# Kernel optimization log

Measured on AMD Instinct MI355X. Metric: run time of the kernel, lower is better.

The kernel has to match this reference:

```python
import jax, jax.numpy as jnp
import numpy as np

B, S, E = 2, 2048, 2048
H, KV, D = 16, 4, 128
G = H // KV  # query heads per kv head
THETA = 10000.0


def setup_inputs() -> dict:
    key = jax.random.key(0)
    ks = jax.random.split(key, 5)
    scale = 0.02
    return {
        "x": jax.random.normal(ks[0], (B, S, E), dtype=jnp.float32),
        "Wq": jax.random.normal(ks[1], (E, H * D), dtype=jnp.float32) * scale,
        "Wk": jax.random.normal(ks[2], (E, KV * D), dtype=jnp.float32) * scale,
        "Wv": jax.random.normal(ks[3], (E, KV * D), dtype=jnp.float32) * scale,
        "Wo": jax.random.normal(ks[4], (E, E), dtype=jnp.float32) * scale,
    }


def _rope_tables(seq_len, head_dim, theta):
    inv_freq = 1.0 / theta ** (jnp.arange(0, head_dim, 2, dtype=jnp.float32) / head_dim)
    t = jnp.arange(seq_len, dtype=jnp.float32)
    freqs = jnp.outer(t, inv_freq)  # [S, D/2]
    cos = jnp.concatenate([jnp.cos(freqs), jnp.cos(freqs)], axis=-1)  # [S, D]
    sin = jnp.concatenate([jnp.sin(freqs), jnp.sin(freqs)], axis=-1)
    return cos, sin


def _apply_rope(x, cos, sin):
    # x: [B, h, S, D]; cos/sin: [S, D] broadcast over batch/heads
    d2 = x.shape[-1] // 2
    x1, x2 = x[..., :d2], x[..., d2:]
    rotated = jnp.concatenate([-x2, x1], axis=-1)
    return x * cos + rotated * sin


def reference(x, Wq, Wk, Wv, Wo):
    b, s, _ = x.shape
    q = (x @ Wq).reshape(b, s, H, D).transpose(0, 2, 1, 3)   # [B,H,S,D]
    k = (x @ Wk).reshape(b, s, KV, D).transpose(0, 2, 1, 3)  # [B,KV,S,D]
    v = (x @ Wv).reshape(b, s, KV, D).transpose(0, 2, 1, 3)

    cos, sin = _rope_tables(s, D, THETA)
    q = _apply_rope(q, cos, sin)
    k = _apply_rope(k, cos, sin)

    # GQA: q head h attends to kv head h // G (repeat_interleave order)
    qg = q.reshape(b, KV, G, s, D)
    scores = jnp.einsum("bkgsd,bktd->bkgst", qg, k) / jnp.sqrt(jnp.asarray(D, x.dtype))
    causal = jnp.tril(jnp.ones((s, s), dtype=bool))
    scores = jnp.where(causal, scores, jnp.asarray(-jnp.inf, scores.dtype))
    attn = jax.nn.softmax(scores, axis=-1)
    out = jnp.einsum("bkgst,bktd->bkgsd", attn, v)  # [B,KV,G,S,D]
    out = out.reshape(b, H, s, D).transpose(0, 2, 1, 3).reshape(b, s, H * D)
    return out @ Wo
```

## Files before the change

kernel.cpp:

```cpp
#include <hip/hip_runtime.h>
#include <stdint.h>

#define B_ 2
#define S_ 2048
#define E_ 2048
#define H_ 16
#define KV_ 4
#define D_ 128
#define G_ (H_ / KV_)
#define M_ (B_ * S_)

typedef unsigned short u16;
typedef unsigned int u32;
typedef __bf16 bf16x8 __attribute__((ext_vector_type(8)));
typedef float f32x4 __attribute__((ext_vector_type(4)));

__device__ __forceinline__ u16 f2bf(float f) {
  __bf16 h = (__bf16)f;
  return *(u16*)&h;
}
__device__ __forceinline__ float bf2f(u16 x) {
  return __uint_as_float(((u32)x) << 16);
}
__device__ __forceinline__ void store_c(u16* p, float v) { *p = f2bf(v); }
__device__ __forceinline__ void store_c(float* p, float v) { *p = v; }

__device__ __forceinline__ void gload_lds16(const u16* g, u16* lds) {
  __builtin_amdgcn_global_load_lds((const __attribute__((address_space(1))) u32*)g,
                                   (__attribute__((address_space(3))) u32*)lds,
                                   16, 0, 0);
}

__global__ __launch_bounds__(256) void convert_fp32_bf16(const float4* __restrict__ x,
                                                         uint2* __restrict__ o, int n4) {
  int i = blockIdx.x * 256 + threadIdx.x;
  if (i >= n4) return;
  float4 v = x[i];
  uint2 r;
  r.x = (u32)f2bf(v.x) | ((u32)f2bf(v.y) << 16);
  r.y = (u32)f2bf(v.z) | ((u32)f2bf(v.w) << 16);
  o[i] = r;
}

__global__ __launch_bounds__(256) void transpose_conv_w(const float* __restrict__ W,
                                                        u16* __restrict__ Wt,
                                                        int Kdim, int Ndim) {
  __shared__ float tile[32][33];
  int n0 = blockIdx.x * 32, k0 = blockIdx.y * 32;
  int tx = threadIdx.x, ty = threadIdx.y;
#pragma unroll
  for (int i = 0; i < 4; i++) {
    int r = ty + i * 8;
    tile[r][tx] = W[(size_t)(k0 + r) * Ndim + n0 + tx];
  }
  __syncthreads();
#pragma unroll
  for (int i = 0; i < 4; i++) {
    int r = ty + i * 8;
    Wt[(size_t)(n0 + r) * Kdim + k0 + tx] = f2bf(tile[tx][r]);
  }
}

__global__ __launch_bounds__(256) void transpose_v(const u16* __restrict__ V,
                                                   u16* __restrict__ Vt) {
  __shared__ u16 tile[32][33];
  int bkv = blockIdx.z;
  int b = bkv / KV_, kv = bkv % KV_;
  int s0 = blockIdx.x * 32, d0 = blockIdx.y * 32;
  int tx = threadIdx.x, ty = threadIdx.y;
#pragma unroll
  for (int i = 0; i < 4; i++) {
    int r = ty + i * 8;
    tile[r][tx] = V[((size_t)((b * S_ + s0 + r) * KV_ + kv)) * D_ + d0 + tx];
  }
  __syncthreads();
#pragma unroll
  for (int i = 0; i < 4; i++) {
    int r = ty + i * 8;
    Vt[((size_t)(b * KV_ + kv) * D_ + d0 + r) * S_ + s0 + tx] = tile[tx][r];
  }
}

__global__ __launch_bounds__(256) void rope_k_repack(const u16* __restrict__ Kin,
                                                     u16* __restrict__ Kp, int total) {
  int idx = blockIdx.x * 256 + threadIdx.x;
  if (idx >= total) return;
  int d = idx & 63;
  int rem = idx >> 6;
  int kv = rem % KV_;
  int row = rem / KV_;
  int b = row >> 11;
  int spos = row & (S_ - 1);
  size_t src = ((size_t)row * KV_ + kv) * D_ + d;
  float x0 = bf2f(Kin[src]);
  float x1 = bf2f(Kin[src + 64]);
  float ang = (float)spos * expf(-0.14391156831212787f * (float)d);
  float sn, cs;
  sincosf(ang, &sn, &cs);
  size_t dst = ((size_t)((b * KV_ + kv) * S_ + spos)) * D_ + d;
  Kp[dst]      = f2bf(x0 * cs - x1 * sn);
  Kp[dst + 64] = f2bf(x1 * cs + x0 * sn);
}

template <typename CT>
__device__ __forceinline__ void gemm256_body(const u16* __restrict__ A,
                                             const u16* __restrict__ Bt,
                                             CT* __restrict__ C,
                                             int Kdim, int Ndim, int m0, int n0) {
  extern __shared__ __align__(16) u16 smem[];
  const int tid  = threadIdx.x;
  const int lane = tid & 63;
  const int wave = tid >> 6;
  const int wm   = wave >> 2;
  const int wn   = wave & 3;
  const int bh   = wn >> 1;
  const int nb   = (wn & 1) * 64;
  const int quad = lane >> 4, lm = lane & 15;

  int soff[2], sldb[2];
#pragma unroll
  for (int i = 0; i < 2; i++) {
    int cc  = i * 512 + tid;
    int row = cc >> 3;
    int q   = (cc & 7) ^ (row & 7);
    soff[i] = row * Kdim + q * 8;
    sldb[i] = (i * 512 + wave * 64) * 8;
  }
  auto STAGE = [&](const u16* g, u16* l) {
    gload_lds16(g + soff[0], l + sldb[0]);
    gload_lds16(g + soff[1], l + sldb[1]);
  };

  int cs0 = ((0 + quad) ^ (lm & 7)) * 8;
  int cs1 = ((4 + quad) ^ (lm & 7)) * 8;

  const u16* Ag = A  + (size_t)m0 * Kdim;
  const u16* Bg = Bt + (size_t)n0 * Kdim;
  const size_t hstep = (size_t)128 * Kdim;

  f32x4 acc[8][4];
  f32x4 zero = {0.f, 0.f, 0.f, 0.f};
#pragma unroll
  for (int m = 0; m < 8; m++)
#pragma unroll
    for (int n = 0; n < 4; n++) acc[m][n] = zero;

  const int NKT = Kdim >> 6;

  STAGE(Bg,             smem + 32768 + 0 * 8192);
  STAGE(Ag,             smem + 0 * 8192);
  STAGE(Ag + hstep,     smem + 1 * 8192);
  STAGE(Bg + hstep,     smem + 32768 + 1 * 8192);
  STAGE(Bg + 64,        smem + 32768 + 2 * 8192);
  STAGE(Ag + 64,        smem + 2 * 8192);
  STAGE(Ag + hstep + 64, smem + 3 * 8192);
  asm volatile("s_waitcnt vmcnt(6)" ::: "memory");
  __builtin_amdgcn_s_barrier();

  for (int kt = 0; kt < NKT; ++kt) {
    const int cur = kt & 1;
    const u16* regA = smem + (cur * 2 + wm) * 8192;
    const u16* regB = smem + 32768 + (cur * 2 + bh) * 8192;
    bf16x8 af[4][2], bf[4][2];

#pragma unroll
    for (int n = 0; n < 4; n++) {
      bf[n][0] = *(const bf16x8*)(regB + (nb + n * 16 + lm) * 64 + cs0);
      bf[n][1] = *(const bf16x8*)(regB + (nb + n * 16 + lm) * 64 + cs1);
    }
#pragma unroll
    for (int m = 0; m < 4; m++) {
      af[m][0] = *(const bf16x8*)(regA + (m * 16 + lm) * 64 + cs0);
      af[m][1] = *(const bf16x8*)(regA + (m * 16 + lm) * 64 + cs1);
    }
    if (kt + 1 < NKT)
      STAGE(Bg + hstep + (size_t)(kt + 1) * 64,
            smem + 32768 + (((kt + 1) & 1) * 2 + 1) * 8192);
    asm volatile("s_waitcnt lgkmcnt(0)" ::: "memory");
    __builtin_amdgcn_s_barrier();
    __builtin_amdgcn_s_setprio(1);
#pragma unroll
    for (int m = 0; m < 4; m++)
#pragma unroll
      for (int n = 0; n < 2; n++) {
        acc[m][n] = __builtin_amdgcn_mfma_f32_16x16x32_bf16(af[m][0], bf[n][0], acc[m][n], 0, 0, 0);
        acc[m][n] = __builtin_amdgcn_mfma_f32_16x16x32_bf16(af[m][1], bf[n][1], acc[m][n], 0, 0, 0);
      }
    __builtin_amdgcn_s_setprio(0);
    __builtin_amdgcn_s_barrier();

    if (kt + 2 < NKT)
      STAGE(Bg + (size_t)(kt + 2) * 64, smem + 32768 + (cur * 2 + 0) * 8192);
    __builtin_amdgcn_s_barrier();
    __builtin_amdgcn_s_setprio(1);
#pragma unroll
    for (int m = 0; m < 4; m++)
#pragma unroll
      for (int n = 2; n < 4; n++) {
        acc[m][n] = __builtin_amdgcn_mfma_f32_16x16x32_bf16(af[m][0], bf[n][0], acc[m][n], 0, 0, 0);
        acc[m][n] = __builtin_amdgcn_mfma_f32_16x16x32_bf16(af[m][1], bf[n][1], acc[m][n], 0, 0, 0);
      }
    __builtin_amdgcn_s_setprio(0);
    __builtin_amdgcn_s_barrier();

#pragma unroll
    for (int m = 0; m < 4; m++) {
      af[m][0] = *(const bf16x8*)(regA + ((m + 4) * 16 + lm) * 64 + cs0);
      af[m][1] = *(const bf16x8*)(regA + ((m + 4) * 16 + lm) * 64 + cs1);
    }
    asm volatile("s_waitcnt lgkmcnt(0)" ::: "memory");
    __builtin_amdgcn_s_barrier();
    __builtin_amdgcn_s_setprio(1);
#pragma unroll
    for (int m = 0; m < 4; m++)
#pragma unroll
      for (int n = 0; n < 2; n++) {
        acc[m + 4][n] = __builtin_amdgcn_mfma_f32_16x16x32_bf16(af[m][0], bf[n][0], acc[m + 4][n], 0, 0, 0);
        acc[m + 4][n] = __builtin_amdgcn_mfma_f32_16x16x32_bf16(af[m][1], bf[n][1], acc[m + 4][n], 0, 0, 0);
      }
    __builtin_amdgcn_s_setprio(0);
    __builtin_amdgcn_s_barrier();

    if (kt + 2 < NKT) {
      STAGE(Ag + (size_t)(kt + 2) * 64,         smem + (cur * 2 + 0) * 8192);
      STAGE(Ag + hstep + (size_t)(kt + 2) * 64, smem + (cur * 2 + 1) * 8192);
    }
    __builtin_amdgcn_s_setprio(1);
#pragma unroll
    for (int m = 0; m < 4; m++)
#pragma unroll
      for (int n = 2; n < 4; n++) {
        acc[m + 4][n] = __builtin_amdgcn_mfma_f32_16x16x32_bf16(af[m][0], bf[n][0], acc[m + 4][n], 0, 0, 0);
        acc[m + 4][n] = __builtin_amdgcn_mfma_f32_16x16x32_bf16(af[m][1], bf[n][1], acc[m + 4][n], 0, 0, 0);
      }
    __builtin_amdgcn_s_setprio(0);
    asm volatile("s_waitcnt vmcnt(6)" ::: "memory");
    __builtin_amdgcn_s_barrier();
  }

#pragma unroll
  for (int m = 0; m < 8; m++) {
    const int row = m0 + wm * 128 + m * 16 + quad * 4;
#pragma unroll
    for (int n = 0; n < 4; n++) {
      const int col = n0 + wn * 64 + n * 16 + lm;
#pragma unroll
      for (int r = 0; r < 4; r++)
        store_c(C + (size_t)(row + r) * Ndim + col, acc[m][n][r]);
    }
  }
}

__global__ __launch_bounds__(512, 2) void gemm256_qkv(const u16* __restrict__ A,
                                                      const u16* __restrict__ WqT,
                                                      const u16* __restrict__ WkT,
                                                      const u16* __restrict__ WvT,
                                                      u16* __restrict__ Qb,
                                                      u16* __restrict__ Kb,
                                                      u16* __restrict__ Vb) {
  int bx = blockIdx.x;
  const u16* Bt;
  u16* C;
  int n0, Ndim;
  if (bx < 8)       { Bt = WqT; C = Qb; n0 = bx * 256;        Ndim = 2048; }
  else if (bx < 10) { Bt = WkT; C = Kb; n0 = (bx - 8) * 256;  Ndim = 512; }
  else              { Bt = WvT; C = Vb; n0 = (bx - 10) * 256; Ndim = 512; }
  gemm256_body<u16>(A, Bt, C, 2048, Ndim, blockIdx.y * 256, n0);
}

__global__ __launch_bounds__(512, 2) void gemm256_wo(const u16* __restrict__ A,
                                                     const u16* __restrict__ Bt,
                                                     float* __restrict__ C) {
  gemm256_body<float>(A, Bt, C, 2048, 2048, blockIdx.y * 256, blockIdx.x * 256);
}

__global__ __launch_bounds__(256, 2) void attn_kernel(const u16* __restrict__ Q,
                                                      const u16* __restrict__ Kp,
                                                      const u16* __restrict__ Vt,
                                                      u16* __restrict__ O) {
  __shared__ __align__(16) u16 Ksh[2][64 * 128];
  __shared__ __align__(16) u16 Vsh[128 * 64];
  __shared__ __align__(16) u16 Psh[4][16 * 64];

  const int tid = threadIdx.x;
  const int lane = tid & 63;
  const int wave = tid >> 6;
  const int quad = lane >> 4, lm = lane & 15;
  const int b = blockIdx.z, h = blockIdx.y;
  const int kh = h / G_;

  const u16* Kbase = Kp + (size_t)(b * KV_ + kh) * S_ * D_;
  const u16* Vbase = Vt + (size_t)(b * KV_ + kh) * D_ * S_;
  u16* pw = &Psh[wave][0];

  int offK[4], offV[4], ldsOff[4];
#pragma unroll
  for (int i = 0; i < 4; i++) {
    int idx = (wave * 4 + i) * 64 + lane;
    int rK = idx >> 4;
    int cK = (idx & 15) ^ (rK & 7);
    offK[i] = rK * 128 + cK * 8;
    int rV = idx >> 3;
    int cV = (idx & 7) ^ (rV & 7);
    offV[i] = rV * S_ + cV * 8;
    ldsOff[i] = (wave * 4 + i) * 512;
  }

  bf16x8 onesb;
#pragma unroll
  for (int j = 0; j < 8; j++) onesb[j] = (__bf16)1.0f;

#pragma unroll
  for (int half = 0; half < 2; half++) {
    const int qi = half ? blockIdx.x : (31 - blockIdx.x);
    const int sq0 = qi * 64;
    const int nT = qi + 1;
    const int wrow = sq0 + wave * 16;

    const int spos = wrow + lm;
    const u16* qptr = Q + ((size_t)(b * S_ + wrow + lm) * H_ + h) * D_;
    bf16x8 qf[4];
#pragma unroll
    for (int ks = 0; ks < 2; ks++) {
      bf16x8 a = *(const bf16x8*)(qptr + ks * 32 + quad * 8);
      bf16x8 c = *(const bf16x8*)(qptr + (ks + 2) * 32 + quad * 8);
#pragma unroll
      for (int j = 0; j < 8; j++) {
        int d = ks * 32 + quad * 8 + j;
        float ang = (float)spos * __expf(-0.14391156831212787f * (float)d);
        float sn, cs;
        sincosf(ang, &sn, &cs);
        float x0 = (float)a[j], x1 = (float)c[j];
        const float scale = 0.08838834764831845f;
        qf[ks][j]     = (__bf16)((x0 * cs - x1 * sn) * scale);
        qf[ks + 2][j] = (__bf16)((x1 * cs + x0 * sn) * scale);
      }
    }

    f32x4 o[8];
    f32x4 lacc = {0.f, 0.f, 0.f, 0.f};
#pragma unroll
    for (int i = 0; i < 8; i++) o[i] = f32x4{0.f, 0.f, 0.f, 0.f};

    __syncthreads();
#pragma unroll
    for (int i = 0; i < 4; i++)
      gload_lds16(Kbase + offK[i], &Ksh[0][ldsOff[i]]);

    for (int t = 0; t < nT; t++) {
      const int sk0 = t << 6;
      const bool act = (sk0 <= wrow + 15);
      __syncthreads();

      if (t + 1 < nT) {
        const u16* kg = Kbase + (size_t)(t + 1) * 64 * 128;
        u16* kb_next = &Ksh[(t + 1) & 1][0];
#pragma unroll
        for (int i = 0; i < 4; i++)
          gload_lds16(kg + offK[i], kb_next + ldsOff[i]);
      }
#pragma unroll
      for (int i = 0; i < 4; i++)
        gload_lds16(Vbase + sk0 + offV[i], &Vsh[ldsOff[i]]);

      f32x4 sc[4];
      if (act) {
        const u16* kbuf = &Ksh[t & 1][0];
#pragma unroll
        for (int nt = 0; nt < 4; nt++) sc[nt] = f32x4{0.f, 0.f, 0.f, 0.f};
#pragma unroll
        for (int ks = 0; ks < 4; ks++) {
#pragma unroll
          for (int nt = 0; nt < 4; nt++) {
            int R = nt * 16 + lm;
            bf16x8 kb = *(const bf16x8*)(kbuf + R * 128 + (((ks * 4 + quad) ^ (R & 7)) * 8));
            sc[nt] = __builtin_amdgcn_mfma_f32_16x16x32_bf16(qf[ks], kb, sc[nt], 0, 0, 0);
          }
        }
#pragma unroll
        for (int nt = 0; nt < 4; nt++)
#pragma unroll
          for (int r = 0; r < 4; r++) {
            float p = __expf(sc[nt][r]);
            int kc = sk0 + nt * 16 + lm;
            int qr = wrow + quad * 4 + r;
            sc[nt][r] = (kc > qr) ? 0.f : p;
          }
#pragma unroll
        for (int nt = 0; nt < 4; nt++)
#pragma unroll
          for (int r = 0; r < 4; r++) {
            int p = quad * 4 + r;
            int c = nt * 2 + (lm >> 3);
            pw[p * 64 + ((c ^ (p & 7)) * 8) + (lm & 7)] = f2bf(sc[nt][r]);
          }
      }

      __syncthreads();

      if (act) {
#pragma unroll
        for (int ks = 0; ks < 2; ks++) {
          int pr = lm;
          bf16x8 pa = *(const bf16x8*)(pw + pr * 64 + (((ks * 4 + quad) ^ (pr & 7)) * 8));
          lacc = __builtin_amdgcn_mfma_f32_16x16x32_bf16(pa, onesb, lacc, 0, 0, 0);
#pragma unroll
          for (int d8 = 0; d8 < 8; d8++) {
            int R = d8 * 16 + lm;
            bf16x8 vb = *(const bf16x8*)(Vsh + R * 64 + (((ks * 4 + quad) ^ (R & 7)) * 8));
            o[d8] = __builtin_amdgcn_mfma_f32_16x16x32_bf16(pa, vb, o[d8], 0, 0, 0);
          }
        }
      }
    }

    float inv[4];
#pragma unroll
    for (int r = 0; r < 4; r++) inv[r] = 1.0f / lacc[r];
#pragma unroll
    for (int d8 = 0; d8 < 8; d8++)
#pragma unroll
      for (int r = 0; r < 4; r++) {
        int srow = wrow + quad * 4 + r;
        O[((size_t)(b * S_ + srow) * H_ + h) * D_ + d8 * 16 + lm] = f2bf(o[d8][r] * inv[r]);
      }
  }
}

extern "C" void kernel_launch(void* const* d_in, const int* in_sizes, int n_in,
                              void* d_out, int out_size, void* d_ws, size_t ws_size,
                              hipStream_t stream) {
  const float* x  = (const float*)d_in[0];
  const float* Wq = (const float*)d_in[1];
  const float* Wk = (const float*)d_in[2];
  const float* Wv = (const float*)d_in[3];
  const float* Wo = (const float*)d_in[4];
  float* out = (float*)d_out;
  char* ws = (char*)d_ws;
  u16* Xb  = (u16*)(ws);
  u16* WqT = (u16*)(ws + (16ull << 20));
  u16* WkT = (u16*)(ws + (24ull << 20));
  u16* WvT = (u16*)(ws + (26ull << 20));
  u16* WoT = (u16*)(ws + (28ull << 20));
  u16* Qb  = (u16*)(ws + (36ull << 20));
  u16* Kb  = (u16*)(ws + (52ull << 20));
  u16* Vb  = (u16*)(ws + (56ull << 20));
  u16* Vt  = (u16*)(ws + (60ull << 20));
  u16* Ob  = (u16*)(ws + (64ull << 20));
  u16* Kp  = (u16*)(ws + (80ull << 20));

  static bool attr_set = false;
  if (!attr_set) {
    hipFuncSetAttribute((const void*)gemm256_qkv,
                        hipFuncAttributeMaxDynamicSharedMemorySize, 131072);
    hipFuncSetAttribute((const void*)gemm256_wo,
                        hipFuncAttributeMaxDynamicSharedMemorySize, 131072);
    attr_set = true;
  }

  dim3 tb32(32, 8);

  convert_fp32_bf16<<<dim3(M_ * E_ / 4 / 256), 256, 0, stream>>>((const float4*)x, (uint2*)Xb, M_ * E_ / 4);
  transpose_conv_w<<<dim3(2048 / 32, 2048 / 32), tb32, 0, stream>>>(Wq, WqT, E_, H_ * D_);
  transpose_conv_w<<<dim3(512 / 32, 2048 / 32), tb32, 0, stream>>>(Wk, WkT, E_, KV_ * D_);
  transpose_conv_w<<<dim3(512 / 32, 2048 / 32), tb32, 0, stream>>>(Wv, WvT, E_, KV_ * D_);
  transpose_conv_w<<<dim3(2048 / 32, 2048 / 32), tb32, 0, stream>>>(Wo, WoT, E_, E_);

  gemm256_qkv<<<dim3(12, M_ / 256), 512, 131072, stream>>>(Xb, WqT, WkT, WvT, Qb, Kb, Vb);

  rope_k_repack<<<dim3(M_ * KV_ * 64 / 256), 256, 0, stream>>>(Kb, Kp, M_ * KV_ * 64);

  transpose_v<<<dim3(S_ / 32, D_ / 32, B_ * KV_), tb32, 0, stream>>>(Vb, Vt);

  attn_kernel<<<dim3(16, H_, B_), 256, 0, stream>>>(Qb, Kp, Vt, Ob);

  gemm256_wo<<<dim3(2048 / 256, M_ / 256), 512, 131072, stream>>>(Ob, WoT, out);
}
```

Measured before the change: 316.5 us.

## Double-buffer V tiles, use explicit waitcnt barriers, and reorder attention grid

The attention loop now double-buffers V in LDS alongside K, so the next K and V tiles are both prefetched while the current tile is computed. The two __syncthreads per iteration become raw s_barrier calls with explicit vmcnt waits, and the barrier between the P write and the PV MFMA is dropped because each wave only reads its own P slice. MFMA sections are wrapped in s_setprio, and the grid is swapped so heads vary fastest, which is meant to let blocks sharing a KV head hit L2 together. In exchange it uses more LDS, and the hand-written waitcnt counts are a correctness risk if the load count changes.

```diff
diff --git a/kernel.cpp b/kernel.cpp
--- a/kernel.cpp
+++ b/kernel.cpp
@@ -279,14 +279,14 @@
                                                       const u16* __restrict__ Vt,
                                                       u16* __restrict__ O) {
   __shared__ __align__(16) u16 Ksh[2][64 * 128];
-  __shared__ __align__(16) u16 Vsh[128 * 64];
+  __shared__ __align__(16) u16 Vsh[2][128 * 64];
   __shared__ __align__(16) u16 Psh[4][16 * 64];
 
   const int tid = threadIdx.x;
   const int lane = tid & 63;
   const int wave = tid >> 6;
   const int quad = lane >> 4, lm = lane & 15;
-  const int b = blockIdx.z, h = blockIdx.y;
+  const int b = blockIdx.z, h = blockIdx.x;
   const int kh = h / G_;
 
   const u16* Kbase = Kp + (size_t)(b * KV_ + kh) * S_ * D_;
@@ -312,7 +312,7 @@
 
 #pragma unroll
   for (int half = 0; half < 2; half++) {
-    const int qi = half ? blockIdx.x : (31 - blockIdx.x);
+    const int qi = half ? blockIdx.y : (31 - blockIdx.y);
     const int sq0 = qi * 64;
     const int nT = qi + 1;
     const int wrow = sq0 + wave * 16;
@@ -343,31 +343,45 @@
     for (int i = 0; i < 8; i++) o[i] = f32x4{0.f, 0.f, 0.f, 0.f};
 
     __syncthreads();
+
 #pragma unroll
     for (int i = 0; i < 4; i++)
       gload_lds16(Kbase + offK[i], &Ksh[0][ldsOff[i]]);
+#pragma unroll
+    for (int i = 0; i < 4; i++)
+      gload_lds16(Vbase + offV[i], &Vsh[0][ldsOff[i]]);
 
     for (int t = 0; t < nT; t++) {
       const int sk0 = t << 6;
       const bool act = (sk0 <= wrow + 15);
-      __syncthreads();
+
+      __builtin_amdgcn_s_barrier();
 
       if (t + 1 < nT) {
         const u16* kg = Kbase + (size_t)(t + 1) * 64 * 128;
+        const u16* vg = Vbase + (t + 1) * 64;
         u16* kb_next = &Ksh[(t + 1) & 1][0];
+        u16* vb_next = &Vsh[(t + 1) & 1][0];
 #pragma unroll
         for (int i = 0; i < 4; i++)
           gload_lds16(kg + offK[i], kb_next + ldsOff[i]);
-      }
-#pragma unroll
-      for (int i = 0; i < 4; i++)
-        gload_lds16(Vbase + sk0 + offV[i], &Vsh[ldsOff[i]]);
-
-      f32x4 sc[4];
+#pragma unroll
+        for (int i = 0; i < 4; i++)
+          gload_lds16(vg + offV[i], vb_next + ldsOff[i]);
+        asm volatile("s_waitcnt vmcnt(8)" ::: "memory");
+      } else {
+        asm volatile("s_waitcnt vmcnt(0)" ::: "memory");
+      }
+
+      __builtin_amdgcn_s_barrier();
+      __builtin_amdgcn_sched_barrier(0);
+
       if (act) {
         const u16* kbuf = &Ksh[t & 1][0];
+        f32x4 sc[4];
 #pragma unroll
         for (int nt = 0; nt < 4; nt++) sc[nt] = f32x4{0.f, 0.f, 0.f, 0.f};
+        __builtin_amdgcn_s_setprio(1);
 #pragma unroll
         for (int ks = 0; ks < 4; ks++) {
 #pragma unroll
@@ -377,6 +391,7 @@
             sc[nt] = __builtin_amdgcn_mfma_f32_16x16x32_bf16(qf[ks], kb, sc[nt], 0, 0, 0);
           }
         }
+        __builtin_amdgcn_s_setprio(0);
 #pragma unroll
         for (int nt = 0; nt < 4; nt++)
 #pragma unroll
@@ -394,11 +409,8 @@
             int c = nt * 2 + (lm >> 3);
             pw[p * 64 + ((c ^ (p & 7)) * 8) + (lm & 7)] = f2bf(sc[nt][r]);
           }
-      }
-
-      __syncthreads();
-
-      if (act) {
+        const u16* vbuf = &Vsh[t & 1][0];
+        __builtin_amdgcn_s_setprio(1);
 #pragma unroll
         for (int ks = 0; ks < 2; ks++) {
           int pr = lm;
@@ -407,10 +419,11 @@
 #pragma unroll
           for (int d8 = 0; d8 < 8; d8++) {
             int R = d8 * 16 + lm;
-            bf16x8 vb = *(const bf16x8*)(Vsh + R * 64 + (((ks * 4 + quad) ^ (R & 7)) * 8));
+            bf16x8 vb = *(const bf16x8*)(vbuf + R * 64 + (((ks * 4 + quad) ^ (R & 7)) * 8));
             o[d8] = __builtin_amdgcn_mfma_f32_16x16x32_bf16(pa, vb, o[d8], 0, 0, 0);
           }
         }
+        __builtin_amdgcn_s_setprio(0);
       }
     }
 
@@ -472,7 +485,7 @@
 
   transpose_v<<<dim3(S_ / 32, D_ / 32, B_ * KV_), tb32, 0, stream>>>(Vb, Vt);
 
-  attn_kernel<<<dim3(16, H_, B_), 256, 0, stream>>>(Qb, Kp, Vt, Ob);
+  attn_kernel<<<dim3(H_, 16, B_), 256, 0, stream>>>(Qb, Kp, Vt, Ob);
 
   gemm256_wo<<<dim3(2048 / 256, M_ / 256), 512, 131072, stream>>>(Ob, WoT, out);
 }
```

Result: no change. 313.6 us (-0.9%).
